# Kernel optimization log

Hardware: AMD Instinct MI355X
Metric: run time of the kernel (lower is better)

The kernel has to match this reference:

```python
import jax, jax.numpy as jnp
import numpy as np
import math

# Constants matching init_kwargs
H = 16            # num_attention_heads
K = 8             # tisa_num_kernels
NUM_AGNOSTIC = 2  # num_position_agnostic_heads
MAX_FV = 512.0
MIN_FV = 8.0
P_EPS = 1e-8
EPS = 1e-8


def _slopes():
    # ALiBi-like geometric slope schedule from the module __init__ (non-learned buffer)
    first = -math.log(P_EPS) / (MIN_FV / 2.0)
    last = -math.log(P_EPS) / (MAX_FV / 2.0)
    aware = H - NUM_AGNOSTIC
    s = first * (last / first) ** (jnp.arange(H, dtype=jnp.float32) / (aware - 1))
    # position-agnostic heads get zero slope
    return s * (jnp.arange(H) < aware).astype(jnp.float32)


def setup_inputs() -> dict:
    key = jax.random.key(0)
    ks = jax.random.split(key, 5)
    B, L, D = 4, 1024, 64
    q = jax.random.normal(ks[0], (B, H, L, D), jnp.float32)
    k = jax.random.normal(ks[1], (B, H, L, D), jnp.float32)
    v = jax.random.normal(ks[2], (B, H, L, D), jnp.float32)
    offsets = jax.random.normal(ks[3], (1, K, H, 1, 1), jnp.float32) * 15.0
    amplitudes = jax.random.normal(ks[4], (1, K, H, 1, 1), jnp.float32) * 0.01
    sharpness = jnp.full((1, K, H, 1, 1), 5.0, jnp.float32)
    bias_param = jnp.ones((1, H, 1, 1), jnp.float32)
    return {"q": q, "k": k, "v": v, "offsets": offsets, "amplitudes": amplitudes,
            "sharpness": sharpness, "bias_param": bias_param}


def reference(q, k, v, offsets, amplitudes, sharpness, bias_param):
    B, Hh, L, D = q.shape
    rel = jnp.arange(-L + 1, L, dtype=q.dtype)            # (2L-1,) relative positions
    slopes = _slopes()                                     # (H,)
    exp_decay = -jnp.abs(rel)[None, :] * slopes[:, None]   # (H, 2L-1)

    off = offsets.reshape(K, Hh, 1)
    amp = amplitudes.reshape(K, Hh, 1)
    sh = sharpness.reshape(K, Hh, 1)
    # sigmoid kernel per (kernel, head, relpos); eval mode -> no dropout
    kernel = jnp.abs(amp) * jax.nn.sigmoid(jnp.sign(amp) * ((rel[None, None, :] - off) / sh))
    ksum = kernel.sum(axis=0)                              # (H, 2L-1)
    bias_rel = jnp.log(ksum + EPS + bias_param.reshape(Hh, 1))
    rel_bias = bias_rel + exp_decay                        # (H, 2L-1)

    # relative -> absolute: bias[i, j] = rel_bias[j - i + L - 1]
    idx = jnp.arange(L)[None, :] - jnp.arange(L)[:, None] + (L - 1)  # (L, L)
    attn_bias = rel_bias[:, idx]                           # (H, L, L)

    scale = 1.0 / jnp.sqrt(jnp.asarray(D, q.dtype))
    scores = jnp.einsum('bhqd,bhkd->bhqk', q, k) * scale + attn_bias[None]
    probs = jax.nn.softmax(scores, axis=-1)
    return jnp.einsum('bhqk,bhkd->bhqd', probs, v)
```

## Files before the change

### kernel.cpp

```cpp
#include <hip/hip_runtime.h>
#include <math.h>

#define Bq 4
#define Hh 16
#define Lq 1024
#define Dd 64
#define Kk 8
#define QT 128
#define KT 128
#define SRk 72
#define SRv 136
#define TB 1152
#define FMAX 8.0f
#define LOG2E 1.44269504f

#define KSZ (KT * SRk * 2)
#define VSZ (Dd * SRv * 2)
#define BOFF (KSZ + VSZ)
#define SMEM_BYTES (BOFF + 4 * TB * 4)

typedef __attribute__((ext_vector_type(8))) short short8;
typedef __attribute__((ext_vector_type(4))) unsigned int u32x4;
typedef __attribute__((ext_vector_type(16))) float f32x16;

__device__ __forceinline__ unsigned int pk2(float a, float b) {
    return __builtin_amdgcn_perm(__float_as_uint(b) + 0x8000u,
                                 __float_as_uint(a) + 0x8000u,
                                 0x07060302u);
}

__device__ __forceinline__ int jperm(int j) {
    return (j & 32) | ((j & 8) << 1) | ((j & 4) << 1) | ((j & 16) >> 2) | (j & 3);
}

__global__ __launch_bounds__(512, 2) void attn_kernel(
    const float* __restrict__ qp, const float* __restrict__ kp,
    const float* __restrict__ vp,
    const float* __restrict__ off, const float* __restrict__ amp,
    const float* __restrict__ sh, const float* __restrict__ bpar,
    float* __restrict__ out)
{
    __shared__ __align__(16) char smem[SMEM_BYTES];
    short* k_s   = (short*)smem;
    short* v_s   = (short*)(smem + KSZ);
    float* bias4 = (float*)(smem + BOFF);

    const int bh = blockIdx.x;
    const int qs = blockIdx.y * QT;
    const int t  = threadIdx.x;
    const int w  = t >> 6;
    const int qw = w >> 1;
    const int sw = w & 1;
    const int lane = t & 63;
    const int l31 = lane & 31;
    const int h5  = lane >> 5;
    const int h   = bh & 15;

    float slope = (h < Hh - 2) ? 4.605170185988092f * exp2f(-6.0f * (float)h / 13.0f) : 0.0f;
    #pragma unroll
    for (int it = 0; it < 3; ++it) {
        int i = it * 512 + t;
        if (i < TB - 1) {
            float rel = (float)(i - 127 - qs);
            float ksum = 0.0f;
            #pragma unroll
            for (int kk = 0; kk < Kk; ++kk) {
                float a = amp[kk * Hh + h];
                float o = off[kk * Hh + h];
                float s = sh[kk * Hh + h];
                float sgn = (a > 0.0f) ? 1.0f : ((a < 0.0f) ? -1.0f : 0.0f);
                ksum += fabsf(a) / (1.0f + __expf(-sgn * (rel - o) / s));
            }
            bias4[i] = (logf(ksum + 1e-8f + bpar[h]) - fabsf(rel) * slope - FMAX) * LOG2E;
        }
    }

    const float QS = 0.125f * LOG2E;
    short8 bq[4];
    const float* qrow = qp + ((size_t)bh * Lq + qs + 32 * qw + l31) * Dd;
    #pragma unroll
    for (int c = 0; c < 4; ++c) {
        float4 x0 = *(const float4*)(qrow + c * 16 + h5 * 8);
        float4 x1 = *(const float4*)(qrow + c * 16 + h5 * 8 + 4);
        u32x4 a;
        a[0] = pk2(x0.x * QS, x0.y * QS);
        a[1] = pk2(x0.z * QS, x0.w * QS);
        a[2] = pk2(x1.x * QS, x1.y * QS);
        a[3] = pk2(x1.z * QS, x1.w * QS);
        bq[c] = __builtin_bit_cast(short8, a);
    }

    const int g  = t >> 4;
    const int cl = t & 15;
    const int c4 = 4 * cl;
    const int jrow = 4 * g;
    const int vcb = 64 * (g >> 4) + jperm(jrow & 63);
    const float* kbase = kp + (size_t)bh * Lq * Dd;
    const float* vbase = vp + (size_t)bh * Lq * Dd;

    float4 kr[4], vr[4];
    #pragma unroll
    for (int u = 0; u < 4; ++u) {
        kr[u] = *(const float4*)(kbase + (size_t)(jrow + u) * Dd + c4);
        vr[u] = *(const float4*)(vbase + (size_t)(jrow + u) * Dd + c4);
    }

    __syncthreads();

    #pragma unroll
    for (int it = 0; it < 3; ++it) {
        int i = it * 512 + t;
        if (i < TB) {
            float b1 = bias4[i + 1 <= TB - 2 ? i + 1 : TB - 2];
            float b2 = bias4[i + 2 <= TB - 2 ? i + 2 : TB - 2];
            float b3 = bias4[i + 3 <= TB - 2 ? i + 3 : TB - 2];
            bias4[TB + i]     = b1;
            bias4[2 * TB + i] = b2;
            bias4[3 * TB + i] = b3;
        }
    }
    #pragma unroll
    for (int u = 0; u < 4; ++u) {
        uint2 kv;
        kv.x = pk2(kr[u].x, kr[u].y);
        kv.y = pk2(kr[u].z, kr[u].w);
        *(uint2*)&k_s[(jrow + u) * SRk + c4] = kv;
    }
    #pragma unroll
    for (int cc = 0; cc < 4; ++cc) {
        int d = c4 + cc;
        uint2 vv;
        vv.x = pk2(((const float*)&vr[0])[cc], ((const float*)&vr[1])[cc]);
        vv.y = pk2(((const float*)&vr[2])[cc], ((const float*)&vr[3])[cc]);
        *(uint2*)&v_s[d * SRv + (vcb ^ (8 * ((d >> 3) & 7)))] = vv;
    }
    __syncthreads();

    f32x16 O0, O1;
    #pragma unroll
    for (int r = 0; r < 16; ++r) { O0[r] = 0.f; O1[r] = 0.f; }
    float l_part = 0.0f;

    const int L0 = 4 * h5 - 32 * qw - l31 + 127;
    const int phi = L0 & 3;
    const float* bcopy = bias4 + phi * TB - phi;

    #pragma unroll 1
    for (int kt = 0; kt < Lq / KT; ++kt) {
        const int ks = kt * KT;

        if (kt < 7) {
            const float* kn = kbase + (size_t)(ks + KT) * Dd;
            const float* vn = vbase + (size_t)(ks + KT) * Dd;
            #pragma unroll
            for (int u = 0; u < 4; ++u) {
                kr[u] = *(const float4*)(kn + (size_t)(jrow + u) * Dd + c4);
                vr[u] = *(const float4*)(vn + (size_t)(jrow + u) * Dd + c4);
            }
        }

        f32x16 S0, S1;
        #pragma unroll
        for (int r = 0; r < 16; ++r) { S0[r] = 0.f; S1[r] = 0.f; }
        #pragma unroll
        for (int c = 0; c < 4; ++c) {
            short8 ak0 = *(const short8*)&k_s[(64 * sw + l31) * SRk + c * 16 + h5 * 8];
            S0 = __builtin_amdgcn_mfma_f32_32x32x16_bf16(ak0, bq[c], S0, 0, 0, 0);
        }
        #pragma unroll
        for (int c = 0; c < 4; ++c) {
            short8 ak1 = *(const short8*)&k_s[(64 * sw + 32 + l31) * SRk + c * 16 + h5 * 8];
            S1 = __builtin_amdgcn_mfma_f32_32x32x16_bf16(ak1, bq[c], S1, 0, 0, 0);
        }

        float lsum = 0.0f;
        #pragma unroll
        for (int p = 0; p < 4; ++p) {
            int base0 = ks + 64 * sw + 8 * p + L0;
            float4 b0 = *(const float4*)(bcopy + base0);
            float4 b1 = *(const float4*)(bcopy + base0 + 32);
            #pragma unroll
            for (int q = 0; q < 4; ++q) {
                int r = 4 * p + q;
                float bq0 = (q == 0) ? b0.x : (q == 1) ? b0.y : (q == 2) ? b0.z : b0.w;
                float bq1 = (q == 0) ? b1.x : (q == 1) ? b1.y : (q == 2) ? b1.z : b1.w;
                float e0 = __builtin_amdgcn_exp2f(S0[r] + bq0);
                float e1 = __builtin_amdgcn_exp2f(S1[r] + bq1);
                S0[r] = e0; S1[r] = e1;
                lsum += e0 + e1;
            }
        }
        l_part += lsum;

        short8 ap[4];
        #pragma unroll
        for (int c = 0; c < 4; ++c) {
            int b = (c & 1) * 4;
            u32x4 a;
            if (c >> 1) {
                a[0] = pk2(S1[b + 0], S1[b + 1]);
                a[1] = pk2(S1[b + 2], S1[b + 3]);
                a[2] = pk2(S1[b + 8], S1[b + 9]);
                a[3] = pk2(S1[b + 10], S1[b + 11]);
            } else {
                a[0] = pk2(S0[b + 0], S0[b + 1]);
                a[1] = pk2(S0[b + 2], S0[b + 3]);
                a[2] = pk2(S0[b + 8], S0[b + 9]);
                a[3] = pk2(S0[b + 10], S0[b + 11]);
            }
            ap[c] = __builtin_bit_cast(short8, a);
        }

        #pragma unroll
        for (int nb = 0; nb < 2; ++nb) {
            int d = nb * 32 + l31;
            int swz = 8 * ((d >> 3) & 7);
            f32x16 acc = nb ? O1 : O0;
            #pragma unroll
            for (int c = 0; c < 4; ++c) {
                short8 bv = *(const short8*)&v_s[d * SRv + 64 * sw + ((c * 16 + h5 * 8) ^ swz)];
                acc = __builtin_amdgcn_mfma_f32_32x32x16_bf16(ap[c], bv, acc, 0, 0, 0);
            }
            if (nb) O1 = acc; else O0 = acc;
        }

        __syncthreads();
        if (kt < 7) {
            #pragma unroll
            for (int u = 0; u < 4; ++u) {
                uint2 kv;
                kv.x = pk2(kr[u].x, kr[u].y);
                kv.y = pk2(kr[u].z, kr[u].w);
                *(uint2*)&k_s[(jrow + u) * SRk + c4] = kv;
            }
            #pragma unroll
            for (int cc = 0; cc < 4; ++cc) {
                int d = c4 + cc;
                uint2 vv;
                vv.x = pk2(((const float*)&vr[0])[cc], ((const float*)&vr[1])[cc]);
                vv.y = pk2(((const float*)&vr[2])[cc], ((const float*)&vr[3])[cc]);
                *(uint2*)&v_s[d * SRv + (vcb ^ (8 * ((d >> 3) & 7)))] = vv;
            }
        }
        __syncthreads();
    }

    l_part += __shfl_xor(l_part, 32);
    float* red = (float*)smem;
    const int rb = (w * 64 + lane) * 17;
    #pragma unroll
    for (int r = 0; r < 16; ++r) red[rb + r] = sw ? O0[r] : O1[r];
    red[rb + 16] = l_part;
    __syncthreads();
    const int pb = ((w ^ 1) * 64 + lane) * 17;
    float inv = 1.0f / (l_part + red[pb + 16]);
    float* ob = out + ((size_t)bh * Lq + qs + 32 * qw) * Dd;
    #pragma unroll
    for (int r = 0; r < 16; ++r) {
        float o = (sw ? O1[r] : O0[r]) + red[pb + r];
        int rowp = (r & 3) + 8 * (r >> 2) + 4 * h5;
        float invp = __shfl(inv, rowp, 32);
        ob[(size_t)rowp * Dd + 32 * sw + l31] = o * invp;
    }
}

extern "C" void kernel_launch(void* const* d_in, const int* in_sizes, int n_in,
                              void* d_out, int out_size, void* d_ws, size_t ws_size,
                              hipStream_t stream) {
    const float* q   = (const float*)d_in[0];
    const float* k   = (const float*)d_in[1];
    const float* v   = (const float*)d_in[2];
    const float* off = (const float*)d_in[3];
    const float* amp = (const float*)d_in[4];
    const float* sh  = (const float*)d_in[5];
    const float* bp  = (const float*)d_in[6];
    float* out = (float*)d_out;

    dim3 grid(Bq * Hh, Lq / QT);
    attn_kernel<<<grid, 512, 0, stream>>>(q, k, v, off, amp, sh, bp, out);
}
```

Measured before the change: 128.8 us.

## Double-buffer K/V tiles in LDS and fold bias into MFMA accumulator init

Splits LDS into two K/V buffers so the next tile is written into the alternate buffer, dropping one of the two __syncthreads per key-tile iteration. The bias is preloaded into the score accumulators before the QK MFMAs, which removes the separate bias add in the softmax loop. To fit both K/V buffers, the shifted bias copies shrink from four to two and are read with float2 loads instead of float4. The larger LDS footprint may reduce occupancy against the __launch_bounds__(512,2) target.

```diff
diff --git a/kernel.cpp b/kernel.cpp
--- a/kernel.cpp
+++ b/kernel.cpp
@@ -14,10 +14,10 @@
 #define FMAX 8.0f
 #define LOG2E 1.44269504f
 
-#define KSZ (KT * SRk * 2)
-#define VSZ (Dd * SRv * 2)
-#define BOFF (KSZ + VSZ)
-#define SMEM_BYTES (BOFF + 4 * TB * 4)
+#define KBUF (KT * SRk * 2)
+#define VBUF (Dd * SRv * 2)
+#define BOFF (2 * (KBUF + VBUF))
+#define SMEM_BYTES (BOFF + 2 * TB * 4)
 
 typedef __attribute__((ext_vector_type(8))) short short8;
 typedef __attribute__((ext_vector_type(4))) unsigned int u32x4;
@@ -41,9 +41,7 @@
     float* __restrict__ out)
 {
     __shared__ __align__(16) char smem[SMEM_BYTES];
-    short* k_s   = (short*)smem;
-    short* v_s   = (short*)(smem + KSZ);
-    float* bias4 = (float*)(smem + BOFF);
+    float* bias2 = (float*)(smem + BOFF);
 
     const int bh = blockIdx.x;
     const int qs = blockIdx.y * QT;
@@ -71,7 +69,7 @@
                 float sgn = (a > 0.0f) ? 1.0f : ((a < 0.0f) ? -1.0f : 0.0f);
                 ksum += fabsf(a) / (1.0f + __expf(-sgn * (rel - o) / s));
             }
-            bias4[i] = (logf(ksum + 1e-8f + bpar[h]) - fabsf(rel) * slope - FMAX) * LOG2E;
+            bias2[i] = (logf(ksum + 1e-8f + bpar[h]) - fabsf(rel) * slope - FMAX) * LOG2E;
         }
     }
 
@@ -110,29 +108,27 @@
     #pragma unroll
     for (int it = 0; it < 3; ++it) {
         int i = it * 512 + t;
-        if (i < TB) {
-            float b1 = bias4[i + 1 <= TB - 2 ? i + 1 : TB - 2];
-            float b2 = bias4[i + 2 <= TB - 2 ? i + 2 : TB - 2];
-            float b3 = bias4[i + 3 <= TB - 2 ? i + 3 : TB - 2];
-            bias4[TB + i]     = b1;
-            bias4[2 * TB + i] = b2;
-            bias4[3 * TB + i] = b3;
-        }
-    }
-    #pragma unroll
-    for (int u = 0; u < 4; ++u) {
-        uint2 kv;
-        kv.x = pk2(kr[u].x, kr[u].y);
-        kv.y = pk2(kr[u].z, kr[u].w);
-        *(uint2*)&k_s[(jrow + u) * SRk + c4] = kv;
-    }
-    #pragma unroll
-    for (int cc = 0; cc < 4; ++cc) {
-        int d = c4 + cc;
-        uint2 vv;
-        vv.x = pk2(((const float*)&vr[0])[cc], ((const float*)&vr[1])[cc]);
-        vv.y = pk2(((const float*)&vr[2])[cc], ((const float*)&vr[3])[cc]);
-        *(uint2*)&v_s[d * SRv + (vcb ^ (8 * ((d >> 3) & 7)))] = vv;
+        if (i < TB)
+            bias2[TB + i] = bias2[i + 1 <= TB - 2 ? i + 1 : TB - 2];
+    }
+    {
+        short* kw = (short*)(smem);
+        short* vw = (short*)(smem + 2 * KBUF);
+        #pragma unroll
+        for (int u = 0; u < 4; ++u) {
+            uint2 kv;
+            kv.x = pk2(kr[u].x, kr[u].y);
+            kv.y = pk2(kr[u].z, kr[u].w);
+            *(uint2*)&kw[(jrow + u) * SRk + c4] = kv;
+        }
+        #pragma unroll
+        for (int cc = 0; cc < 4; ++cc) {
+            int d = c4 + cc;
+            uint2 vv;
+            vv.x = pk2(((const float*)&vr[0])[cc], ((const float*)&vr[1])[cc]);
+            vv.y = pk2(((const float*)&vr[2])[cc], ((const float*)&vr[3])[cc]);
+            *(uint2*)&vw[d * SRv + (vcb ^ (8 * ((d >> 3) & 7)))] = vv;
+        }
     }
     __syncthreads();
 
@@ -142,12 +138,15 @@
     float l_part = 0.0f;
 
     const int L0 = 4 * h5 - 32 * qw - l31 + 127;
-    const int phi = L0 & 3;
-    const float* bcopy = bias4 + phi * TB - phi;
+    const int phi = L0 & 1;
+    const float* bcopy = bias2 + phi * TB - phi;
 
     #pragma unroll 1
     for (int kt = 0; kt < Lq / KT; ++kt) {
         const int ks = kt * KT;
+        const int cur = kt & 1;
+        const short* kc = (const short*)(smem + cur * KBUF);
+        const short* vc = (const short*)(smem + 2 * KBUF + cur * VBUF);
 
         if (kt < 7) {
             const float* kn = kbase + (size_t)(ks + KT) * Dd;
@@ -161,34 +160,36 @@
 
         f32x16 S0, S1;
         #pragma unroll
-        for (int r = 0; r < 16; ++r) { S0[r] = 0.f; S1[r] = 0.f; }
-        #pragma unroll
-        for (int c = 0; c < 4; ++c) {
-            short8 ak0 = *(const short8*)&k_s[(64 * sw + l31) * SRk + c * 16 + h5 * 8];
-            S0 = __builtin_amdgcn_mfma_f32_32x32x16_bf16(ak0, bq[c], S0, 0, 0, 0);
-        }
-        #pragma unroll
-        for (int c = 0; c < 4; ++c) {
-            short8 ak1 = *(const short8*)&k_s[(64 * sw + 32 + l31) * SRk + c * 16 + h5 * 8];
-            S1 = __builtin_amdgcn_mfma_f32_32x32x16_bf16(ak1, bq[c], S1, 0, 0, 0);
-        }
-
-        float lsum = 0.0f;
-        #pragma unroll
         for (int p = 0; p < 4; ++p) {
             int base0 = ks + 64 * sw + 8 * p + L0;
-            float4 b0 = *(const float4*)(bcopy + base0);
-            float4 b1 = *(const float4*)(bcopy + base0 + 32);
-            #pragma unroll
-            for (int q = 0; q < 4; ++q) {
-                int r = 4 * p + q;
-                float bq0 = (q == 0) ? b0.x : (q == 1) ? b0.y : (q == 2) ? b0.z : b0.w;
-                float bq1 = (q == 0) ? b1.x : (q == 1) ? b1.y : (q == 2) ? b1.z : b1.w;
-                float e0 = __builtin_amdgcn_exp2f(S0[r] + bq0);
-                float e1 = __builtin_amdgcn_exp2f(S1[r] + bq1);
-                S0[r] = e0; S1[r] = e1;
-                lsum += e0 + e1;
-            }
+            float2 a0 = *(const float2*)(bcopy + base0);
+            float2 a1 = *(const float2*)(bcopy + base0 + 2);
+            float2 a2 = *(const float2*)(bcopy + base0 + 32);
+            float2 a3 = *(const float2*)(bcopy + base0 + 34);
+            S0[4 * p + 0] = a0.x; S0[4 * p + 1] = a0.y;
+            S0[4 * p + 2] = a1.x; S0[4 * p + 3] = a1.y;
+            S1[4 * p + 0] = a2.x; S1[4 * p + 1] = a2.y;
+            S1[4 * p + 2] = a3.x; S1[4 * p + 3] = a3.y;
+        }
+
+        #pragma unroll
+        for (int c = 0; c < 4; ++c) {
+            short8 ak0 = *(const short8*)&kc[(64 * sw + l31) * SRk + c * 16 + h5 * 8];
+            S0 = __builtin_amdgcn_mfma_f32_32x32x16_bf16(ak0, bq[c], S0, 0, 0, 0);
+        }
+        #pragma unroll
+        for (int c = 0; c < 4; ++c) {
+            short8 ak1 = *(const short8*)&kc[(64 * sw + 32 + l31) * SRk + c * 16 + h5 * 8];
+            S1 = __builtin_amdgcn_mfma_f32_32x32x16_bf16(ak1, bq[c], S1, 0, 0, 0);
+        }
+
+        float lsum = 0.0f;
+        #pragma unroll
+        for (int r = 0; r < 16; ++r) {
+            float e0 = __builtin_amdgcn_exp2f(S0[r]);
+            float e1 = __builtin_amdgcn_exp2f(S1[r]);
+            S0[r] = e0; S1[r] = e1;
+            lsum += e0 + e1;
         }
         l_part += lsum;
 
@@ -218,20 +219,21 @@
             f32x16 acc = nb ? O1 : O0;
             #pragma unroll
             for (int c = 0; c < 4; ++c) {
-                short8 bv = *(const short8*)&v_s[d * SRv + 64 * sw + ((c * 16 + h5 * 8) ^ swz)];
+                short8 bv = *(const short8*)&vc[d * SRv + 64 * sw + ((c * 16 + h5 * 8) ^ swz)];
                 acc = __builtin_amdgcn_mfma_f32_32x32x16_bf16(ap[c], bv, acc, 0, 0, 0);
             }
             if (nb) O1 = acc; else O0 = acc;
         }
 
-        __syncthreads();
         if (kt < 7) {
+            short* kw = (short*)(smem + (cur ^ 1) * KBUF);
+            short* vw = (short*)(smem + 2 * KBUF + (cur ^ 1) * VBUF);
             #pragma unroll
             for (int u = 0; u < 4; ++u) {
                 uint2 kv;
                 kv.x = pk2(kr[u].x, kr[u].y);
                 kv.y = pk2(kr[u].z, kr[u].w);
-                *(uint2*)&k_s[(jrow + u) * SRk + c4] = kv;
+                *(uint2*)&kw[(jrow + u) * SRk + c4] = kv;
             }
             #pragma unroll
             for (int cc = 0; cc < 4; ++cc) {
@@ -239,7 +241,7 @@
                 uint2 vv;
                 vv.x = pk2(((const float*)&vr[0])[cc], ((const float*)&vr[1])[cc]);
                 vv.y = pk2(((const float*)&vr[2])[cc], ((const float*)&vr[3])[cc]);
-                *(uint2*)&v_s[d * SRv + (vcb ^ (8 * ((d >> 3) & 7)))] = vv;
+                *(uint2*)&vw[d * SRv + (vcb ^ (8 * ((d >> 3) & 7)))] = vv;
             }
         }
         __syncthreads();
```

Result: no change. 130.7 us (+1.5%).

## Fold bias into MFMA accumulator, compute row sums via MFMA, use hardware bf16 pack

Applied to the files above, without the earlier changes.

Initializes the QK^T MFMA accumulators with the positional bias so the separate bias add disappears. The per-row softmax denominator is now computed by an extra MFMA against a ones vector instead of scalar adds and shuffles. The manual bf16 rounding via perm is replaced with the v_cvt_pk_bf16_f32 instruction, and s_setprio brackets the MFMA sections. This removes VALU work from the exp stage, but adds MFMA work, another accumulator's registers and extra epilogue syncs. The row sum now uses bf16-rounded probabilities, consistent with the values fed to the PV product.

```diff
diff --git a/kernel.cpp b/kernel.cpp
--- a/kernel.cpp
+++ b/kernel.cpp
@@ -29,6 +29,12 @@
                                  0x07060302u);
 }
 
+__device__ __forceinline__ unsigned int cvtpk(float a, float b) {
+    unsigned int r;
+    asm("v_cvt_pk_bf16_f32 %0, %1, %2" : "=v"(r) : "v"(a), "v"(b));
+    return r;
+}
+
 __device__ __forceinline__ int jperm(int j) {
     return (j & 32) | ((j & 8) << 1) | ((j & 4) << 1) | ((j & 16) >> 2) | (j & 3);
 }
@@ -122,24 +128,26 @@
     #pragma unroll
     for (int u = 0; u < 4; ++u) {
         uint2 kv;
-        kv.x = pk2(kr[u].x, kr[u].y);
-        kv.y = pk2(kr[u].z, kr[u].w);
+        kv.x = cvtpk(kr[u].x, kr[u].y);
+        kv.y = cvtpk(kr[u].z, kr[u].w);
         *(uint2*)&k_s[(jrow + u) * SRk + c4] = kv;
     }
     #pragma unroll
     for (int cc = 0; cc < 4; ++cc) {
         int d = c4 + cc;
         uint2 vv;
-        vv.x = pk2(((const float*)&vr[0])[cc], ((const float*)&vr[1])[cc]);
-        vv.y = pk2(((const float*)&vr[2])[cc], ((const float*)&vr[3])[cc]);
+        vv.x = cvtpk(((const float*)&vr[0])[cc], ((const float*)&vr[1])[cc]);
+        vv.y = cvtpk(((const float*)&vr[2])[cc], ((const float*)&vr[3])[cc]);
         *(uint2*)&v_s[d * SRv + (vcb ^ (8 * ((d >> 3) & 7)))] = vv;
     }
     __syncthreads();
 
-    f32x16 O0, O1;
-    #pragma unroll
-    for (int r = 0; r < 16; ++r) { O0[r] = 0.f; O1[r] = 0.f; }
-    float l_part = 0.0f;
+    f32x16 O0, O1, Lacc;
+    #pragma unroll
+    for (int r = 0; r < 16; ++r) { O0[r] = 0.f; O1[r] = 0.f; Lacc[r] = 0.f; }
+    short8 ones;
+    #pragma unroll
+    for (int e = 0; e < 8; ++e) ones[e] = (short)0x3F80;
 
     const int L0 = 4 * h5 - 32 * qw - l31 + 127;
     const int phi = L0 & 3;
@@ -160,37 +168,35 @@
         }
 
         f32x16 S0, S1;
-        #pragma unroll
-        for (int r = 0; r < 16; ++r) { S0[r] = 0.f; S1[r] = 0.f; }
-        #pragma unroll
-        for (int c = 0; c < 4; ++c) {
-            short8 ak0 = *(const short8*)&k_s[(64 * sw + l31) * SRk + c * 16 + h5 * 8];
-            S0 = __builtin_amdgcn_mfma_f32_32x32x16_bf16(ak0, bq[c], S0, 0, 0, 0);
-        }
-        #pragma unroll
-        for (int c = 0; c < 4; ++c) {
-            short8 ak1 = *(const short8*)&k_s[(64 * sw + 32 + l31) * SRk + c * 16 + h5 * 8];
-            S1 = __builtin_amdgcn_mfma_f32_32x32x16_bf16(ak1, bq[c], S1, 0, 0, 0);
-        }
-
-        float lsum = 0.0f;
         #pragma unroll
         for (int p = 0; p < 4; ++p) {
             int base0 = ks + 64 * sw + 8 * p + L0;
             float4 b0 = *(const float4*)(bcopy + base0);
             float4 b1 = *(const float4*)(bcopy + base0 + 32);
-            #pragma unroll
-            for (int q = 0; q < 4; ++q) {
-                int r = 4 * p + q;
-                float bq0 = (q == 0) ? b0.x : (q == 1) ? b0.y : (q == 2) ? b0.z : b0.w;
-                float bq1 = (q == 0) ? b1.x : (q == 1) ? b1.y : (q == 2) ? b1.z : b1.w;
-                float e0 = __builtin_amdgcn_exp2f(S0[r] + bq0);
-                float e1 = __builtin_amdgcn_exp2f(S1[r] + bq1);
-                S0[r] = e0; S1[r] = e1;
-                lsum += e0 + e1;
-            }
-        }
-        l_part += lsum;
+            S0[4 * p + 0] = b0.x; S0[4 * p + 1] = b0.y;
+            S0[4 * p + 2] = b0.z; S0[4 * p + 3] = b0.w;
+            S1[4 * p + 0] = b1.x; S1[4 * p + 1] = b1.y;
+            S1[4 * p + 2] = b1.z; S1[4 * p + 3] = b1.w;
+        }
+
+        __builtin_amdgcn_s_setprio(1);
+        #pragma unroll
+        for (int c = 0; c < 4; ++c) {
+            short8 ak0 = *(const short8*)&k_s[(64 * sw + l31) * SRk + c * 16 + h5 * 8];
+            S0 = __builtin_amdgcn_mfma_f32_32x32x16_bf16(ak0, bq[c], S0, 0, 0, 0);
+        }
+        #pragma unroll
+        for (int c = 0; c < 4; ++c) {
+            short8 ak1 = *(const short8*)&k_s[(64 * sw + 32 + l31) * SRk + c * 16 + h5 * 8];
+            S1 = __builtin_amdgcn_mfma_f32_32x32x16_bf16(ak1, bq[c], S1, 0, 0, 0);
+        }
+        __builtin_amdgcn_s_setprio(0);
+
+        #pragma unroll
+        for (int r = 0; r < 16; ++r) {
+            S0[r] = __builtin_amdgcn_exp2f(S0[r]);
+            S1[r] = __builtin_amdgcn_exp2f(S1[r]);
+        }
 
         short8 ap[4];
         #pragma unroll
@@ -198,19 +204,20 @@
             int b = (c & 1) * 4;
             u32x4 a;
             if (c >> 1) {
-                a[0] = pk2(S1[b + 0], S1[b + 1]);
-                a[1] = pk2(S1[b + 2], S1[b + 3]);
-                a[2] = pk2(S1[b + 8], S1[b + 9]);
-                a[3] = pk2(S1[b + 10], S1[b + 11]);
+                a[0] = cvtpk(S1[b + 0], S1[b + 1]);
+                a[1] = cvtpk(S1[b + 2], S1[b + 3]);
+                a[2] = cvtpk(S1[b + 8], S1[b + 9]);
+                a[3] = cvtpk(S1[b + 10], S1[b + 11]);
             } else {
-                a[0] = pk2(S0[b + 0], S0[b + 1]);
-                a[1] = pk2(S0[b + 2], S0[b + 3]);
-                a[2] = pk2(S0[b + 8], S0[b + 9]);
-                a[3] = pk2(S0[b + 10], S0[b + 11]);
+                a[0] = cvtpk(S0[b + 0], S0[b + 1]);
+                a[1] = cvtpk(S0[b + 2], S0[b + 3]);
+                a[2] = cvtpk(S0[b + 8], S0[b + 9]);
+                a[3] = cvtpk(S0[b + 10], S0[b + 11]);
             }
             ap[c] = __builtin_bit_cast(short8, a);
         }
 
+        __builtin_amdgcn_s_setprio(1);
         #pragma unroll
         for (int nb = 0; nb < 2; ++nb) {
             int d = nb * 32 + l31;
@@ -223,44 +230,51 @@
             }
             if (nb) O1 = acc; else O0 = acc;
         }
+        #pragma unroll
+        for (int c = 0; c < 4; ++c)
+            Lacc = __builtin_amdgcn_mfma_f32_32x32x16_bf16(ap[c], ones, Lacc, 0, 0, 0);
+        __builtin_amdgcn_s_setprio(0);
 
         __syncthreads();
         if (kt < 7) {
             #pragma unroll
             for (int u = 0; u < 4; ++u) {
                 uint2 kv;
-                kv.x = pk2(kr[u].x, kr[u].y);
-                kv.y = pk2(kr[u].z, kr[u].w);
+                kv.x = cvtpk(kr[u].x, kr[u].y);
+                kv.y = cvtpk(kr[u].z, kr[u].w);
                 *(uint2*)&k_s[(jrow + u) * SRk + c4] = kv;
             }
             #pragma unroll
             for (int cc = 0; cc < 4; ++cc) {
                 int d = c4 + cc;
                 uint2 vv;
-                vv.x = pk2(((const float*)&vr[0])[cc], ((const float*)&vr[1])[cc]);
-                vv.y = pk2(((const float*)&vr[2])[cc], ((const float*)&vr[3])[cc]);
+                vv.x = cvtpk(((const float*)&vr[0])[cc], ((const float*)&vr[1])[cc]);
+                vv.y = cvtpk(((const float*)&vr[2])[cc], ((const float*)&vr[3])[cc]);
                 *(uint2*)&v_s[d * SRv + (vcb ^ (8 * ((d >> 3) & 7)))] = vv;
             }
         }
         __syncthreads();
     }
 
-    l_part += __shfl_xor(l_part, 32);
     float* red = (float*)smem;
     const int rb = (w * 64 + lane) * 17;
+    const int pb = ((w ^ 1) * 64 + lane) * 17;
     #pragma unroll
     for (int r = 0; r < 16; ++r) red[rb + r] = sw ? O0[r] : O1[r];
-    red[rb + 16] = l_part;
-    __syncthreads();
-    const int pb = ((w ^ 1) * 64 + lane) * 17;
-    float inv = 1.0f / (l_part + red[pb + 16]);
+    __syncthreads();
+    float ost[16];
+    #pragma unroll
+    for (int r = 0; r < 16; ++r) ost[r] = (sw ? O1[r] : O0[r]) + red[pb + r];
+    __syncthreads();
+    #pragma unroll
+    for (int r = 0; r < 16; ++r) red[rb + r] = Lacc[r];
+    __syncthreads();
     float* ob = out + ((size_t)bh * Lq + qs + 32 * qw) * Dd;
     #pragma unroll
     for (int r = 0; r < 16; ++r) {
-        float o = (sw ? O1[r] : O0[r]) + red[pb + r];
+        float inv = 1.0f / (Lacc[r] + red[pb + r]);
         int rowp = (r & 3) + 8 * (r >> 2) + 4 * h5;
-        float invp = __shfl(inv, rowp, 32);
-        ob[(size_t)rowp * Dd + 32 * sw + l31] = o * invp;
+        ob[(size_t)rowp * Dd + 32 * sw + l31] = ost[r] * inv;
     }
 }
 
```

Result: no change. 128.2 us (-0.5%).
